# Performance work log

Measured on AMD Instinct MI355X. Metric: run time of the kernel, lower is better.

The kernel has to match this reference:

```python
import jax, jax.numpy as jnp
import numpy as np

V, E, H, C, M, CLS = 32000, 300, 512, 256, 512, 1
B, T = 64, 128
NEG = -1e9


def setup_inputs() -> dict:
    key = jax.random.key(0)
    ks = jax.random.split(key, 16)
    u = lambda k, shape, r: jax.random.uniform(k, shape, jnp.float32, -r, r)
    klstm = 1.0 / np.sqrt(H)
    inp = {
        "s1": jax.random.randint(ks[0], (B, T), 0, V, dtype=jnp.int32),
        "s2": jax.random.randint(ks[1], (B, T), 0, V, dtype=jnp.int32),
        "s1_length": jax.random.randint(ks[2], (B,), 1, T + 1, dtype=jnp.int32),
        "s2_length": jax.random.randint(ks[3], (B,), 1, T + 1, dtype=jnp.int32),
        "s1_h0": jnp.zeros((2, B, H), jnp.float32),
        "s1_c0": jnp.zeros((2, B, H), jnp.float32),
        "s2_h0": jnp.zeros((2, B, H), jnp.float32),
        "s2_c0": jnp.zeros((2, B, H), jnp.float32),
        "emb": jax.random.normal(ks[4], (V, E), jnp.float32) * 0.1,
        "Wih_f": u(ks[5], (4 * H, E), klstm),
        "Whh_f": u(ks[6], (4 * H, H), klstm),
        "b_f": u(ks[7], (4 * H,), klstm),
        "Wih_b": u(ks[8], (4 * H, E), klstm),
        "Whh_b": u(ks[9], (4 * H, H), klstm),
        "b_b": u(ks[10], (4 * H,), klstm),
        "S1W": u(ks[11], (C, 2 * H), 0.1),
        "S2W": u(ks[12], (1, C), 0.1),
        "mlpW": u(ks[13], (M, 4 * H), 0.1),
        "mlpb": jnp.zeros((M,), jnp.float32),
        "outW": u(ks[14], (CLS, M), 0.1),
        "outb": jnp.zeros((CLS,), jnp.float32),
    }
    return inp


def lstm(x, h0, c0, Wih, Whh, b):
    # x: [B,T,E] -> outputs [B,T,H]; PyTorch gate order i,f,g,o
    xW = jnp.einsum("bte,ge->btg", x, Wih) + b  # [B,T,4H]

    def step(carry, xw):
        h, c = carry
        g = xw + h @ Whh.T
        i, f, gg, o = jnp.split(g, 4, axis=-1)
        c = jax.nn.sigmoid(f) * c + jax.nn.sigmoid(i) * jnp.tanh(gg)
        h = jax.nn.sigmoid(o) * jnp.tanh(c)
        return (h, c), h

    _, hs = jax.lax.scan(step, (h0, c0), jnp.swapaxes(xW, 0, 1))
    return jnp.swapaxes(hs, 0, 1)


def encode(tokens, lens, h0, c0, emb, Wih_f, Whh_f, b_f, Wih_b, Whh_b, b_b, S1W, S2W):
    x = emb[tokens]  # [B,T,E]
    t = jnp.arange(tokens.shape[1])
    # reverse-within-valid-length indices (pack/pad semantics for bwd direction)
    idx = jnp.where(t[None, :] < lens[:, None], lens[:, None] - 1 - t[None, :], t[None, :])
    out_f = lstm(x, h0[0], c0[0], Wih_f, Whh_f, b_f)
    x_rev = jnp.take_along_axis(x, idx[:, :, None], axis=1)
    out_b = lstm(x_rev, h0[1], c0[1], Wih_b, Whh_b, b_b)
    out_b = jnp.take_along_axis(out_b, idx[:, :, None], axis=1)
    Hout = jnp.concatenate([out_f, out_b], axis=-1)  # [B,T,2H]
    # attention pooling: S2(tanh(S1(H))), softmax over valid positions
    scores = jnp.einsum("btc,c->bt", jnp.tanh(jnp.einsum("btd,cd->btc", Hout, S1W)), S2W[0])
    scores = jnp.where(t[None, :] < lens[:, None], scores, NEG)
    attn = jax.nn.softmax(scores, axis=1)
    return jnp.einsum("bt,btd->bd", attn, Hout)  # [B,2H]


def reference(s1, s2, s1_length, s2_length, s1_h0, s1_c0, s2_h0, s2_c0, emb,
              Wih_f, Whh_f, b_f, Wih_b, Whh_b, b_b, S1W, S2W, mlpW, mlpb, outW, outb):
    r1 = encode(s1, s1_length, s1_h0, s1_c0, emb, Wih_f, Whh_f, b_f, Wih_b, Whh_b, b_b, S1W, S2W)
    r2 = encode(s2, s2_length, s2_h0, s2_c0, emb, Wih_f, Whh_f, b_f, Wih_b, Whh_b, b_b, S1W, S2W)
    merged = jnp.concatenate([r1 + r2, (r1 - r2) ** 2], axis=1)  # [B,4H]
    out_mlp = merged @ mlpW.T + mlpb  # no activation, per original
    return jax.nn.sigmoid(out_mlp @ outW.T + outb)  # [B,CLS]
```

## Files before the change

kernel.cpp:

```cpp
#include <hip/hip_runtime.h>
#include <hip/hip_bf16.h>

#define B_  64
#define T_  128
#define E_  300
#define EP  320
#define H_  512
#define G4  2048
#define R_  128
#define C_  256
#define M_  512
#define TS  (T_ + 1)
#define NB  256

typedef short bf16x8 __attribute__((ext_vector_type(8)));
typedef float f32x4  __attribute__((ext_vector_type(4)));
#define MFMA(a, b, c) __builtin_amdgcn_mfma_f32_16x16x32_bf16((a), (b), (c), 0, 0, 0)

__device__ __forceinline__ float fsig(float x) { return 1.0f / (1.0f + __expf(-x)); }
__device__ __forceinline__ float ftanh(float x) {
    float a = fminf(fabsf(x), 15.0f);
    float e = __expf(2.0f * a);
    return copysignf((e - 1.0f) / (e + 1.0f), x);
}
__device__ __forceinline__ ushort f2bf(float f) {
    __hip_bfloat16 h = __float2bfloat16(f);
    return *reinterpret_cast<ushort*>(&h);
}
__device__ __forceinline__ float bf2f(ushort u) {
    __hip_bfloat16 h = *reinterpret_cast<__hip_bfloat16*>(&u);
    return __bfloat162float(h);
}

__global__ __launch_bounds__(256) void k_cvt(const float* __restrict__ src,
                                             ushort* __restrict__ dst,
                                             int sk, int dk)
{
    const int r = blockIdx.x;
    for (int c = threadIdx.x; c < dk; c += 256)
        dst[(long)r * dk + c] = (c < sk) ? f2bf(src[(long)r * sk + c]) : (ushort)0;
}

__global__ __launch_bounds__(256) void k_init(
    const float* __restrict__ s1_h0, const float* __restrict__ s2_h0,
    ushort* __restrict__ hfB, ushort* __restrict__ hbB)
{
    const int r = blockIdx.x;
    const int rl = (r < B_) ? r : r - B_;
    const float* h0 = (r < B_) ? s1_h0 : s2_h0;
    for (int j = threadIdx.x; j < H_; j += 256) {
        hfB[(long)r * TS * H_ + j] = f2bf(h0[(long)0 * B_ * H_ + (long)rl * H_ + j]);
        hbB[(long)r * TS * H_ + j] = f2bf(h0[(long)1 * B_ * H_ + (long)rl * H_ + j]);
    }
}

__global__ __launch_bounds__(256) void k_embed_mfma(
    const int* __restrict__ s1, const int* __restrict__ s2,
    const int* __restrict__ l1, const int* __restrict__ l2,
    const ushort* __restrict__ embB,
    const ushort* __restrict__ WihBf, const ushort* __restrict__ WihBb,
    const float* __restrict__ b_f, const float* __restrict__ b_b,
    ushort* __restrict__ xf, ushort* __restrict__ xb)
{
    const int dir = blockIdx.z;
    const int r   = blockIdx.y >> 1;
    const int t0  = (blockIdx.y & 1) * 64;
    const int N0  = blockIdx.x * 128;
    const int L   = (r < B_) ? l1[r] : l2[r - B_];
    if (L <= t0) return;

    const int tid = threadIdx.x;
    const int lane = tid & 63, w = tid >> 6;
    const int wm = w & 1, wn = w >> 1;
    const int l15 = lane & 15, q8 = (lane >> 4) * 8;

    __shared__ int toks[64];
    __shared__ __align__(16) ushort As[64][40];
    __shared__ __align__(16) ushort Bs[128][40];

    if (tid < 64) {
        int t  = t0 + tid;
        int tt = dir ? ((t < L) ? (L - 1 - t) : t) : t;
        toks[tid] = (r < B_) ? s1[r * T_ + tt] : s2[(r - B_) * T_ + tt];
    }
    __syncthreads();

    const ushort* Wih  = dir ? WihBb : WihBf;
    const float*  bias = dir ? b_b : b_f;

    f32x4 acc[2][4] = {};

    for (int k0 = 0; k0 < EP; k0 += 32) {
        {
            int row = tid >> 2, seg = tid & 3;
            *(uint4*)&As[row][seg * 8] =
                *(const uint4*)&embB[(long)toks[row] * EP + k0 + seg * 8];
        }
#pragma unroll
        for (int p = 0; p < 2; ++p) {
            int u = tid + p * 256;
            int row = u >> 2, seg = u & 3;
            *(uint4*)&Bs[row][seg * 8] =
                *(const uint4*)&Wih[(long)(N0 + row) * EP + k0 + seg * 8];
        }
        __syncthreads();
        bf16x8 af[2], bfr[4];
#pragma unroll
        for (int mt = 0; mt < 2; ++mt)
            af[mt] = *(const bf16x8*)&As[wm * 32 + mt * 16 + l15][q8];
#pragma unroll
        for (int nt = 0; nt < 4; ++nt)
            bfr[nt] = *(const bf16x8*)&Bs[wn * 64 + nt * 16 + l15][q8];
#pragma unroll
        for (int mt = 0; mt < 2; ++mt)
#pragma unroll
            for (int nt = 0; nt < 4; ++nt)
                acc[mt][nt] = MFMA(af[mt], bfr[nt], acc[mt][nt]);
        __syncthreads();
    }

    ushort* xout = dir ? xb : xf;
#pragma unroll
    for (int mt = 0; mt < 2; ++mt) {
        int m = r * T_ + t0 + wm * 32 + mt * 16 + (lane >> 4) * 4;
#pragma unroll
        for (int nt = 0; nt < 4; ++nt) {
            int col = N0 + wn * 64 + nt * 16 + l15;
            float bv = bias[col];
#pragma unroll
            for (int rg = 0; rg < 4; ++rg)
                xout[(long)(m + rg) * G4 + col] = f2bf(acc[mt][nt][rg] + bv);
        }
    }
}

__global__ __launch_bounds__(256) void k_recur(
    const ushort* __restrict__ xf, const ushort* __restrict__ xb,
    ushort* __restrict__ hfB, ushort* __restrict__ hbB,
    const ushort* __restrict__ WhhBf, const ushort* __restrict__ WhhBb,
    const float* __restrict__ s1_c0, const float* __restrict__ s2_c0,
    int* __restrict__ bar)
{
    const int bx = blockIdx.x;
    const int s  = bx >> 7;
    const int rb = (bx >> 5) & 3;
    const int jb = bx & 31;
    const int r0 = rb * 32, j0 = jb * 16;
    const int grp0 = bx & ~31;

    const ushort* xW  = s ? xb : xf;
    const ushort* Whh = s ? WhhBb : WhhBf;
    ushort* hB = s ? hbB : hfB;

    const int tid = threadIdx.x;
    const int lane = tid & 63;
    const int g = tid >> 6;
    const int l15 = lane & 15, q8 = (lane >> 4) * 8;

    __shared__ __align__(16) ushort As[32][520];
    __shared__ float Gs[4][32][18];

    int* flags = bar;

    bf16x8 bfr[16];
    {
        const ushort* brow = &Whh[((long)g * H_ + j0 + l15) * H_];
#pragma unroll
        for (int ks = 0; ks < 16; ++ks)
            bfr[ks] = *(const bf16x8*)&brow[ks * 32 + q8];
    }

    const int rr = tid >> 3, jj = (tid & 7) * 2;
    const int rg_ = r0 + rr;
    const int rl  = (rg_ < B_) ? rg_ : rg_ - B_;
    const float* c0p = (rg_ < B_) ? s1_c0 : s2_c0;
    float c_0 = c0p[(long)s * B_ * H_ + (long)rl * H_ + j0 + jj];
    float c_1 = c0p[(long)s * B_ * H_ + (long)rl * H_ + j0 + jj + 1];

    const int arow = tid >> 3, aseg = tid & 7;
    const int swz = ((aseg + arow) & 7) * 8;

    for (int t = 0; t < T_; ++t) {
        uint xw[4];
        const long xbase = ((long)rg_ * T_ + t) * G4 + j0 + jj;
#pragma unroll
        for (int gg = 0; gg < 4; ++gg)
            xw[gg] = *(const uint*)&xW[xbase + gg * H_];

        if (t) {
            __syncthreads();
            if (tid == 0)
                __hip_atomic_store(&flags[bx * 32], t, __ATOMIC_RELAXED,
                                   __HIP_MEMORY_SCOPE_AGENT);
            if (tid < 32)
                while (__hip_atomic_load(&flags[(grp0 + tid) * 32],
                                         __ATOMIC_RELAXED,
                                         __HIP_MEMORY_SCOPE_AGENT) < t)
                    __builtin_amdgcn_s_sleep(1);
            __syncthreads();
        }

        const ushort* hrow = &hB[((long)(r0 + arow) * TS + t) * H_ + aseg * 8];
        uint4 av[8];
#pragma unroll
        for (int sl = 0; sl < 8; ++sl) {
            const unsigned long long* p8 =
                (const unsigned long long*)(hrow + sl * 64);
            unsigned long long lo = __hip_atomic_load(p8, __ATOMIC_RELAXED,
                                                      __HIP_MEMORY_SCOPE_AGENT);
            unsigned long long hi = __hip_atomic_load(p8 + 1, __ATOMIC_RELAXED,
                                                      __HIP_MEMORY_SCOPE_AGENT);
            av[sl].x = (uint)lo; av[sl].y = (uint)(lo >> 32);
            av[sl].z = (uint)hi; av[sl].w = (uint)(hi >> 32);
        }

#pragma unroll
        for (int sl = 0; sl < 8; ++sl)
            *(uint4*)&As[arow][sl * 64 + swz] = av[sl];
        __syncthreads();

        f32x4 acc0 = {}, acc1 = {};
#pragma unroll
        for (int ks = 0; ks < 16; ++ks) {
            const int e  = ks * 32 + q8;
            const int sl = e >> 6;
            const int c  = (e >> 3) & 7;
            bf16x8 a0 = *(const bf16x8*)&As[l15][sl * 64 + (((c + l15) & 7) << 3)];
            bf16x8 a1 = *(const bf16x8*)&As[16 + l15][sl * 64 + (((c + l15) & 7) << 3)];
            acc0 = MFMA(a0, bfr[ks], acc0);
            acc1 = MFMA(a1, bfr[ks], acc1);
        }

#pragma unroll
        for (int rg2 = 0; rg2 < 4; ++rg2) {
            Gs[g][(lane >> 4) * 4 + rg2][l15]      = acc0[rg2];
            Gs[g][16 + (lane >> 4) * 4 + rg2][l15] = acc1[rg2];
        }
        __syncthreads();

        float gi0 = Gs[0][rr][jj]     + bf2f((ushort)(xw[0] & 0xffff));
        float gi1 = Gs[0][rr][jj + 1] + bf2f((ushort)(xw[0] >> 16));
        float gf0 = Gs[1][rr][jj]     + bf2f((ushort)(xw[1] & 0xffff));
        float gf1 = Gs[1][rr][jj + 1] + bf2f((ushort)(xw[1] >> 16));
        float gg0 = Gs[2][rr][jj]     + bf2f((ushort)(xw[2] & 0xffff));
        float gg1 = Gs[2][rr][jj + 1] + bf2f((ushort)(xw[2] >> 16));
        float go0 = Gs[3][rr][jj]     + bf2f((ushort)(xw[3] & 0xffff));
        float go1 = Gs[3][rr][jj + 1] + bf2f((ushort)(xw[3] >> 16));

        c_0 = fsig(gf0) * c_0 + fsig(gi0) * ftanh(gg0);
        c_1 = fsig(gf1) * c_1 + fsig(gi1) * ftanh(gg1);
        float h0 = fsig(go0) * ftanh(c_0);
        float h1 = fsig(go1) * ftanh(c_1);

        uint hp = (uint)f2bf(h0) | ((uint)f2bf(h1) << 16);
        __hip_atomic_store((uint*)&hB[((long)rg_ * TS + t + 1) * H_ + j0 + jj],
                           hp, __ATOMIC_RELAXED, __HIP_MEMORY_SCOPE_AGENT);
    }
}

__global__ __launch_bounds__(256) void k_attn_mfma(
    const ushort* __restrict__ hfB, const ushort* __restrict__ hbB,
    const int* __restrict__ l1, const int* __restrict__ l2,
    const ushort* __restrict__ S1WB, float* __restrict__ U)
{
    const int r  = blockIdx.y >> 1;
    const int t0 = (blockIdx.y & 1) * 64;
    const int N0 = blockIdx.x * 64;
    const int L  = (r < B_) ? l1[r] : l2[r - B_];
    if (L <= t0) return;

    const int tid = threadIdx.x;
    const int lane = tid & 63, w = tid >> 6;
    const int wm = w & 1, wn = w >> 1;
    const int l15 = lane & 15, q8 = (lane >> 4) * 8;

    __shared__ __align__(16) ushort As[64][72];
    __shared__ __align__(16) ushort Bs[64][72];

    f32x4 acc[2][2] = {};

    for (int k0 = 0; k0 < 2 * H_; k0 += 64) {
#pragma unroll
        for (int p = 0; p < 2; ++p) {
            int u = tid + p * 256;
            int row = u >> 3, seg = u & 7;
            int tpos = t0 + row;
            int k = k0 + seg * 8;
            long idx;
            const ushort* src;
            if (k0 < H_) {
                src = hfB; idx = ((long)r * TS + tpos + 1) * H_ + k;
            } else {
                int tt = (tpos < L) ? (L - 1 - tpos) : tpos;
                src = hbB; idx = ((long)r * TS + tt + 1) * H_ + (k - H_);
            }
            *(uint4*)&As[row][seg * 8] = *(const uint4*)&src[idx];
        }
#pragma unroll
        for (int p = 0; p < 2; ++p) {
            int u = tid + p * 256;
            int row = u >> 3, seg = u & 7;
            *(uint4*)&Bs[row][seg * 8] =
                *(const uint4*)&S1WB[(long)(N0 + row) * (2 * H_) + k0 + seg * 8];
        }
        __syncthreads();
#pragma unroll
        for (int ks = 0; ks < 2; ++ks) {
            bf16x8 a0 = *(const bf16x8*)&As[wm * 32 + l15][ks * 32 + q8];
            bf16x8 a1 = *(const bf16x8*)&As[wm * 32 + 16 + l15][ks * 32 + q8];
            bf16x8 b0 = *(const bf16x8*)&Bs[wn * 32 + l15][ks * 32 + q8];
            bf16x8 b1 = *(const bf16x8*)&Bs[wn * 32 + 16 + l15][ks * 32 + q8];
            acc[0][0] = MFMA(a0, b0, acc[0][0]);
            acc[0][1] = MFMA(a0, b1, acc[0][1]);
            acc[1][0] = MFMA(a1, b0, acc[1][0]);
            acc[1][1] = MFMA(a1, b1, acc[1][1]);
        }
        __syncthreads();
    }
#pragma unroll
    for (int mt = 0; mt < 2; ++mt) {
        int m = r * T_ + t0 + wm * 32 + mt * 16 + (lane >> 4) * 4;
#pragma unroll
        for (int nt = 0; nt < 2; ++nt) {
            int col = N0 + wn * 32 + nt * 16 + l15;
#pragma unroll
            for (int rg = 0; rg < 4; ++rg)
                U[(long)(m + rg) * C_ + col] = ftanh(acc[mt][nt][rg]);
        }
    }
}

__global__ __launch_bounds__(256) void k_attn_pool(
    const ushort* __restrict__ hfB, const ushort* __restrict__ hbB,
    const float* __restrict__ U, const float* __restrict__ S2W,
    const int* __restrict__ l1, const int* __restrict__ l2,
    float* __restrict__ pooled)
{
    const int r = blockIdx.x;
    const int L = (r < B_) ? l1[r] : l2[r - B_];
    const int tid = threadIdx.x;
    const int lane = tid & 63, w = tid >> 6;

    __shared__ float att[T_];

    for (int tt = w; tt < T_; tt += 4) {
        float p = 0.0f;
        if (tt < L) {
            const float* u = &U[(long)(r * T_ + tt) * C_];
            p = u[lane] * S2W[lane] + u[lane + 64] * S2W[lane + 64]
              + u[lane + 128] * S2W[lane + 128] + u[lane + 192] * S2W[lane + 192];
            for (int off = 32; off; off >>= 1) p += __shfl_down(p, off);
        }
        if (lane == 0) att[tt] = p;
    }
    __syncthreads();

    float mx = -1e30f;
    for (int tt = 0; tt < L; ++tt) mx = fmaxf(mx, att[tt]);
    __syncthreads();
    if (tid < T_) att[tid] = (tid < L) ? __expf(att[tid] - mx) : 0.0f;
    __syncthreads();
    float sum = 0.0f;
    for (int tt = 0; tt < L; ++tt) sum += att[tt];
    float inv = 1.0f / sum;

    for (int d = tid; d < 2 * H_; d += 256) {
        float a = 0.0f;
        for (int tt = 0; tt < L; ++tt) {
            float hv = (d < H_)
                ? bf2f(hfB[((long)r * TS + tt + 1) * H_ + d])
                : bf2f(hbB[((long)r * TS + (L - tt)) * H_ + (d - H_)]);
            a += att[tt] * hv;
        }
        pooled[(long)r * (2 * H_) + d] = a * inv;
    }
}

__global__ __launch_bounds__(256) void k_mlp1(
    const float* __restrict__ pooled,
    const float* __restrict__ mlpW, const float* __restrict__ mlpb,
    float* __restrict__ om)
{
    const int mg = blockIdx.x;
    const int b  = blockIdx.y;
    const int tid = threadIdx.x;
    const int lane = tid & 63, w = tid >> 6;

    __shared__ __align__(16) float sm[2048];

#pragma unroll
    for (int it = 0; it < 8; ++it) {
        int d = tid + it * 256;
        float v;
        if (d < 1024) {
            v = pooled[(long)b * 1024 + d] + pooled[(long)(B_ + b) * 1024 + d];
        } else {
            int dd = d - 1024;
            float x = pooled[(long)b * 1024 + dd] - pooled[(long)(B_ + b) * 1024 + dd];
            v = x * x;
        }
        sm[d] = v;
    }
    __syncthreads();

    for (int i = 0; i < 16; ++i) {
        int mm = mg * 64 + w * 16 + i;
        const float* wrow = &mlpW[(long)mm * 2048];
        float ax = 0.f, ay = 0.f, az = 0.f, aw = 0.f;
#pragma unroll
        for (int it = 0; it < 8; ++it) {
            int k = it * 256 + lane * 4;
            float4 wv = *(const float4*)&wrow[k];
            float4 sv = *(const float4*)&sm[k];
            ax += wv.x * sv.x; ay += wv.y * sv.y;
            az += wv.z * sv.z; aw += wv.w * sv.w;
        }
        float ssum = (ax + ay) + (az + aw);
        for (int off = 32; off; off >>= 1) ssum += __shfl_down(ssum, off);
        if (lane == 0) om[(long)b * M_ + mm] = ssum + mlpb[mm];
    }
}

__global__ __launch_bounds__(256) void k_final(
    const float* __restrict__ om,
    const float* __restrict__ outW, const float* __restrict__ outb,
    float* __restrict__ out)
{
    const int b = blockIdx.x;
    const int tid = threadIdx.x;
    __shared__ float red[256];
    float p = om[(long)b * M_ + tid] * outW[tid]
            + om[(long)b * M_ + 256 + tid] * outW[256 + tid];
    red[tid] = p;
    __syncthreads();
    for (int off = 128; off > 0; off >>= 1) {
        if (tid < off) red[tid] += red[tid + off];
        __syncthreads();
    }
    if (tid == 0) out[b] = 1.0f / (1.0f + __expf(-(red[0] + outb[0])));
}

extern "C" void kernel_launch(void* const* d_in, const int* in_sizes, int n_in,
                              void* d_out, int out_size, void* d_ws, size_t ws_size,
                              hipStream_t stream)
{
    const int*   s1    = (const int*)d_in[0];
    const int*   s2    = (const int*)d_in[1];
    const int*   l1    = (const int*)d_in[2];
    const int*   l2    = (const int*)d_in[3];
    const float* s1_h0 = (const float*)d_in[4];
    const float* s1_c0 = (const float*)d_in[5];
    const float* s2_h0 = (const float*)d_in[6];
    const float* s2_c0 = (const float*)d_in[7];
    const float* emb   = (const float*)d_in[8];
    const float* Wih_f = (const float*)d_in[9];
    const float* Whh_f = (const float*)d_in[10];
    const float* b_f   = (const float*)d_in[11];
    const float* Wih_b = (const float*)d_in[12];
    const float* Whh_b = (const float*)d_in[13];
    const float* b_b   = (const float*)d_in[14];
    const float* S1W   = (const float*)d_in[15];
    const float* S2W   = (const float*)d_in[16];
    const float* mlpW  = (const float*)d_in[17];
    const float* mlpb  = (const float*)d_in[18];
    const float* outW  = (const float*)d_in[19];
    const float* outb  = (const float*)d_in[20];
    float* out = (float*)d_out;

    ushort* p16 = (ushort*)d_ws;
    ushort* embB  = p16;  p16 += (long)32000 * EP;
    ushort* WihBf = p16;  p16 += (long)G4 * EP;
    ushort* WihBb = p16;  p16 += (long)G4 * EP;
    ushort* WhhBf = p16;  p16 += (long)G4 * H_;
    ushort* WhhBb = p16;  p16 += (long)G4 * H_;
    ushort* S1WB  = p16;  p16 += (long)C_ * 2 * H_;
    ushort* xf    = p16;  p16 += (long)R_ * T_ * G4;
    ushort* xb    = p16;  p16 += (long)R_ * T_ * G4;
    ushort* hfB   = p16;  p16 += (long)R_ * TS * H_;
    ushort* hbB   = p16;  p16 += (long)R_ * TS * H_;
    float* pf = (float*)p16;
    float* U      = pf;   pf += (long)R_ * T_ * C_;
    float* pooled = pf;   pf += (long)R_ * 2 * H_;
    float* om     = pf;   pf += (long)B_ * M_;
    int*   bar    = (int*)pf;

    hipMemsetAsync(bar, 0, 64 * 1024, stream);

    k_cvt<<<32000, 256, 0, stream>>>(emb,   embB,  E_, EP);
    k_cvt<<<G4,    256, 0, stream>>>(Wih_f, WihBf, E_, EP);
    k_cvt<<<G4,    256, 0, stream>>>(Wih_b, WihBb, E_, EP);
    k_cvt<<<G4,    256, 0, stream>>>(Whh_f, WhhBf, H_, H_);
    k_cvt<<<G4,    256, 0, stream>>>(Whh_b, WhhBb, H_, H_);
    k_cvt<<<C_,    256, 0, stream>>>(S1W,   S1WB,  2 * H_, 2 * H_);
    k_init<<<R_, 256, 0, stream>>>(s1_h0, s2_h0, hfB, hbB);

    k_embed_mfma<<<dim3(16, 256, 2), 256, 0, stream>>>(
        s1, s2, l1, l2, embB, WihBf, WihBb, b_f, b_b, xf, xb);

    k_recur<<<NB, 256, 0, stream>>>(xf, xb, hfB, hbB, WhhBf, WhhBb,
                                    s1_c0, s2_c0, bar);

    k_attn_mfma<<<dim3(4, 256), 256, 0, stream>>>(hfB, hbB, l1, l2, S1WB, U);
    k_attn_pool<<<R_, 256, 0, stream>>>(hfB, hbB, U, S2W, l1, l2, pooled);

    k_mlp1<<<dim3(8, B_), 256, 0, stream>>>(pooled, mlpW, mlpb, om);
    k_final<<<B_, 256, 0, stream>>>(om, outW, outb, out);
}
```

Measured before the change: 841.3 us.

## Halve recurrence grid with wider column tiles, merge conversion launches, vectorize pooling

The persistent LSTM recurrence kernel now runs 128 blocks instead of 256. Each block covers 32 hidden columns with a 2x2 MFMA tile and keeps twice the Whh fragments in registers. This halves the number of blocks in each step's spin-wait barrier group and the number of redundant h-state loads, but raises register pressure and per-block work. The six weight-conversion launches are merged into one kernel, and the attention pooling loads two bf16 values per load.

```diff
diff --git a/kernel.cpp b/kernel.cpp
--- a/kernel.cpp
+++ b/kernel.cpp
@@ -11,7 +11,7 @@
 #define C_  256
 #define M_  512
 #define TS  (T_ + 1)
-#define NB  256
+#define NB  128
 
 typedef short bf16x8 __attribute__((ext_vector_type(8)));
 typedef float f32x4  __attribute__((ext_vector_type(4)));
@@ -32,11 +32,24 @@
     return __bfloat162float(h);
 }
 
-__global__ __launch_bounds__(256) void k_cvt(const float* __restrict__ src,
-                                             ushort* __restrict__ dst,
-                                             int sk, int dk)
-{
-    const int r = blockIdx.x;
+__global__ __launch_bounds__(256) void k_cvt_all(
+    const float* __restrict__ emb,
+    const float* __restrict__ Wih_f, const float* __restrict__ Wih_b,
+    const float* __restrict__ Whh_f, const float* __restrict__ Whh_b,
+    const float* __restrict__ S1W,
+    ushort* __restrict__ embB,
+    ushort* __restrict__ WihBf, ushort* __restrict__ WihBb,
+    ushort* __restrict__ WhhBf, ushort* __restrict__ WhhBb,
+    ushort* __restrict__ S1WB)
+{
+    int b = blockIdx.x;
+    const float* src; ushort* dst; int r, sk, dk;
+    if (b < 32000)      { src = emb;   dst = embB;  r = b;          sk = E_;    dk = EP; }
+    else if (b < 34048) { src = Wih_f; dst = WihBf; r = b - 32000;  sk = E_;    dk = EP; }
+    else if (b < 36096) { src = Wih_b; dst = WihBb; r = b - 34048;  sk = E_;    dk = EP; }
+    else if (b < 38144) { src = Whh_f; dst = WhhBf; r = b - 36096;  sk = H_;    dk = H_; }
+    else if (b < 40192) { src = Whh_b; dst = WhhBb; r = b - 38144;  sk = H_;    dk = H_; }
+    else                { src = S1W;   dst = S1WB;  r = b - 40192;  sk = 2*H_;  dk = 2*H_; }
     for (int c = threadIdx.x; c < dk; c += 256)
         dst[(long)r * dk + c] = (c < sk) ? f2bf(src[(long)r * sk + c]) : (ushort)0;
 }
@@ -142,11 +155,11 @@
     int* __restrict__ bar)
 {
     const int bx = blockIdx.x;
-    const int s  = bx >> 7;
-    const int rb = (bx >> 5) & 3;
-    const int jb = bx & 31;
-    const int r0 = rb * 32, j0 = jb * 16;
-    const int grp0 = bx & ~31;
+    const int s  = bx >> 6;
+    const int rb = (bx >> 4) & 3;
+    const int jb = bx & 15;
+    const int r0 = rb * 32, j0 = jb * 32;
+    const int grp0 = bx & ~15;
 
     const ushort* xW  = s ? xb : xf;
     const ushort* Whh = s ? WhhBb : WhhBf;
@@ -158,41 +171,44 @@
     const int l15 = lane & 15, q8 = (lane >> 4) * 8;
 
     __shared__ __align__(16) ushort As[32][520];
-    __shared__ float Gs[4][32][18];
+    __shared__ float Gs[4][32][33];
 
     int* flags = bar;
 
-    bf16x8 bfr[16];
-    {
-        const ushort* brow = &Whh[((long)g * H_ + j0 + l15) * H_];
+    bf16x8 bfr[2][16];
+#pragma unroll
+    for (int nt = 0; nt < 2; ++nt) {
+        const ushort* brow = &Whh[((long)g * H_ + j0 + nt * 16 + l15) * H_];
 #pragma unroll
         for (int ks = 0; ks < 16; ++ks)
-            bfr[ks] = *(const bf16x8*)&brow[ks * 32 + q8];
-    }
-
-    const int rr = tid >> 3, jj = (tid & 7) * 2;
+            bfr[nt][ks] = *(const bf16x8*)&brow[ks * 32 + q8];
+    }
+
+    const int rr = tid >> 3, jj = (tid & 7) * 4;
     const int rg_ = r0 + rr;
     const int rl  = (rg_ < B_) ? rg_ : rg_ - B_;
     const float* c0p = (rg_ < B_) ? s1_c0 : s2_c0;
-    float c_0 = c0p[(long)s * B_ * H_ + (long)rl * H_ + j0 + jj];
-    float c_1 = c0p[(long)s * B_ * H_ + (long)rl * H_ + j0 + jj + 1];
+    float cst[4];
+#pragma unroll
+    for (int cc = 0; cc < 4; ++cc)
+        cst[cc] = c0p[(long)s * B_ * H_ + (long)rl * H_ + j0 + jj + cc];
 
     const int arow = tid >> 3, aseg = tid & 7;
     const int swz = ((aseg + arow) & 7) * 8;
 
     for (int t = 0; t < T_; ++t) {
-        uint xw[4];
+        uint2 xw[4];
         const long xbase = ((long)rg_ * T_ + t) * G4 + j0 + jj;
 #pragma unroll
         for (int gg = 0; gg < 4; ++gg)
-            xw[gg] = *(const uint*)&xW[xbase + gg * H_];
+            xw[gg] = *(const uint2*)&xW[xbase + gg * H_];
 
         if (t) {
             __syncthreads();
             if (tid == 0)
                 __hip_atomic_store(&flags[bx * 32], t, __ATOMIC_RELAXED,
                                    __HIP_MEMORY_SCOPE_AGENT);
-            if (tid < 32)
+            if (tid < 16)
                 while (__hip_atomic_load(&flags[(grp0 + tid) * 32],
                                          __ATOMIC_RELAXED,
                                          __HIP_MEMORY_SCOPE_AGENT) < t)
@@ -219,7 +235,7 @@
             *(uint4*)&As[arow][sl * 64 + swz] = av[sl];
         __syncthreads();
 
-        f32x4 acc0 = {}, acc1 = {};
+        f32x4 acc[2][2] = {};
 #pragma unroll
         for (int ks = 0; ks < 16; ++ks) {
             const int e  = ks * 32 + q8;
@@ -227,34 +243,44 @@
             const int c  = (e >> 3) & 7;
             bf16x8 a0 = *(const bf16x8*)&As[l15][sl * 64 + (((c + l15) & 7) << 3)];
             bf16x8 a1 = *(const bf16x8*)&As[16 + l15][sl * 64 + (((c + l15) & 7) << 3)];
-            acc0 = MFMA(a0, bfr[ks], acc0);
-            acc1 = MFMA(a1, bfr[ks], acc1);
-        }
-
-#pragma unroll
-        for (int rg2 = 0; rg2 < 4; ++rg2) {
-            Gs[g][(lane >> 4) * 4 + rg2][l15]      = acc0[rg2];
-            Gs[g][16 + (lane >> 4) * 4 + rg2][l15] = acc1[rg2];
-        }
-        __syncthreads();
-
-        float gi0 = Gs[0][rr][jj]     + bf2f((ushort)(xw[0] & 0xffff));
-        float gi1 = Gs[0][rr][jj + 1] + bf2f((ushort)(xw[0] >> 16));
-        float gf0 = Gs[1][rr][jj]     + bf2f((ushort)(xw[1] & 0xffff));
-        float gf1 = Gs[1][rr][jj + 1] + bf2f((ushort)(xw[1] >> 16));
-        float gg0 = Gs[2][rr][jj]     + bf2f((ushort)(xw[2] & 0xffff));
-        float gg1 = Gs[2][rr][jj + 1] + bf2f((ushort)(xw[2] >> 16));
-        float go0 = Gs[3][rr][jj]     + bf2f((ushort)(xw[3] & 0xffff));
-        float go1 = Gs[3][rr][jj + 1] + bf2f((ushort)(xw[3] >> 16));
-
-        c_0 = fsig(gf0) * c_0 + fsig(gi0) * ftanh(gg0);
-        c_1 = fsig(gf1) * c_1 + fsig(gi1) * ftanh(gg1);
-        float h0 = fsig(go0) * ftanh(c_0);
-        float h1 = fsig(go1) * ftanh(c_1);
-
-        uint hp = (uint)f2bf(h0) | ((uint)f2bf(h1) << 16);
-        __hip_atomic_store((uint*)&hB[((long)rg_ * TS + t + 1) * H_ + j0 + jj],
-                           hp, __ATOMIC_RELAXED, __HIP_MEMORY_SCOPE_AGENT);
+            acc[0][0] = MFMA(a0, bfr[0][ks], acc[0][0]);
+            acc[0][1] = MFMA(a0, bfr[1][ks], acc[0][1]);
+            acc[1][0] = MFMA(a1, bfr[0][ks], acc[1][0]);
+            acc[1][1] = MFMA(a1, bfr[1][ks], acc[1][1]);
+        }
+
+#pragma unroll
+        for (int mt = 0; mt < 2; ++mt)
+#pragma unroll
+            for (int nt = 0; nt < 2; ++nt)
+#pragma unroll
+                for (int rg2 = 0; rg2 < 4; ++rg2)
+                    Gs[g][mt * 16 + (lane >> 4) * 4 + rg2][nt * 16 + l15] =
+                        acc[mt][nt][rg2];
+        __syncthreads();
+
+        ushort hp[4];
+#pragma unroll
+        for (int cc = 0; cc < 4; ++cc) {
+            uint xv0 = (cc < 2) ? xw[0].x : xw[0].y;
+            uint xv1 = (cc < 2) ? xw[1].x : xw[1].y;
+            uint xv2 = (cc < 2) ? xw[2].x : xw[2].y;
+            uint xv3 = (cc < 2) ? xw[3].x : xw[3].y;
+            int sh = (cc & 1) * 16;
+            float gi = Gs[0][rr][jj + cc] + bf2f((ushort)(xv0 >> sh));
+            float gf = Gs[1][rr][jj + cc] + bf2f((ushort)(xv1 >> sh));
+            float gg = Gs[2][rr][jj + cc] + bf2f((ushort)(xv2 >> sh));
+            float go = Gs[3][rr][jj + cc] + bf2f((ushort)(xv3 >> sh));
+            cst[cc] = fsig(gf) * cst[cc] + fsig(gi) * ftanh(gg);
+            hp[cc] = f2bf(fsig(go) * ftanh(cst[cc]));
+        }
+        unsigned long long pk = (unsigned long long)hp[0]
+                              | ((unsigned long long)hp[1] << 16)
+                              | ((unsigned long long)hp[2] << 32)
+                              | ((unsigned long long)hp[3] << 48);
+        __hip_atomic_store(
+            (unsigned long long*)&hB[((long)rg_ * TS + t + 1) * H_ + j0 + jj],
+            pk, __ATOMIC_RELAXED, __HIP_MEMORY_SCOPE_AGENT);
     }
 }
 
@@ -364,15 +390,27 @@
     for (int tt = 0; tt < L; ++tt) sum += att[tt];
     float inv = 1.0f / sum;
 
-    for (int d = tid; d < 2 * H_; d += 256) {
-        float a = 0.0f;
-        for (int tt = 0; tt < L; ++tt) {
-            float hv = (d < H_)
-                ? bf2f(hfB[((long)r * TS + tt + 1) * H_ + d])
-                : bf2f(hbB[((long)r * TS + (L - tt)) * H_ + (d - H_)]);
-            a += att[tt] * hv;
-        }
-        pooled[(long)r * (2 * H_) + d] = a * inv;
+    for (int p = tid; p < 512; p += 256) {
+        float a0 = 0.0f, a1 = 0.0f;
+        if (p < 256) {
+            int d = p * 2;
+            for (int tt = 0; tt < L; ++tt) {
+                uint hv = *(const uint*)&hfB[((long)r * TS + tt + 1) * H_ + d];
+                a0 += att[tt] * bf2f((ushort)(hv & 0xffff));
+                a1 += att[tt] * bf2f((ushort)(hv >> 16));
+            }
+            pooled[(long)r * (2 * H_) + d]     = a0 * inv;
+            pooled[(long)r * (2 * H_) + d + 1] = a1 * inv;
+        } else {
+            int d = (p - 256) * 2;
+            for (int tt = 0; tt < L; ++tt) {
+                uint hv = *(const uint*)&hbB[((long)r * TS + (L - tt)) * H_ + d];
+                a0 += att[tt] * bf2f((ushort)(hv & 0xffff));
+                a1 += att[tt] * bf2f((ushort)(hv >> 16));
+            }
+            pooled[(long)r * (2 * H_) + H_ + d]     = a0 * inv;
+            pooled[(long)r * (2 * H_) + H_ + d + 1] = a1 * inv;
+        }
     }
 }
 
@@ -486,12 +524,8 @@
 
     hipMemsetAsync(bar, 0, 64 * 1024, stream);
 
-    k_cvt<<<32000, 256, 0, stream>>>(emb,   embB,  E_, EP);
-    k_cvt<<<G4,    256, 0, stream>>>(Wih_f, WihBf, E_, EP);
-    k_cvt<<<G4,    256, 0, stream>>>(Wih_b, WihBb, E_, EP);
-    k_cvt<<<G4,    256, 0, stream>>>(Whh_f, WhhBf, H_, H_);
-    k_cvt<<<G4,    256, 0, stream>>>(Whh_b, WhhBb, H_, H_);
-    k_cvt<<<C_,    256, 0, stream>>>(S1W,   S1WB,  2 * H_, 2 * H_);
+    k_cvt_all<<<40448, 256, 0, stream>>>(emb, Wih_f, Wih_b, Whh_f, Whh_b, S1W,
+                                         embB, WihBf, WihBb, WhhBf, WhhBb, S1WB);
     k_init<<<R_, 256, 0, stream>>>(s1_h0, s2_h0, hfB, hbB);
 
     k_embed_mfma<<<dim3(16, 256, 2), 256, 0, stream>>>(
```

Result: no change. 827.1 us (-1.7%).
